# Kernel tuning notes

Hardware: AMD Instinct MI355X
Metric: run time of the kernel (lower is better)

Reference implementation:

```python
import jax, jax.numpy as jnp
import numpy as np
from jax import lax


def fps(xyz, npoints):
    """Furthest point sampling. xyz: [B,N,3] -> indices [B,npoints] (int32).
    Matches the standard PointNet++ CUDA kernel: first index is 0, then
    iteratively pick the point furthest from the selected set."""
    B, N, _ = xyz.shape
    first = jnp.zeros((B,), jnp.int32)
    d0 = jnp.sum((xyz - xyz[:, :1]) ** 2, axis=-1)  # [B,N] dist^2 to point 0

    def body(dists, _):
        idx = jnp.argmax(dists, axis=-1).astype(jnp.int32)  # [B]
        p = jnp.take_along_axis(xyz, idx[:, None, None].astype(jnp.int32), axis=1)  # [B,1,3]
        d = jnp.sum((xyz - p) ** 2, axis=-1)  # [B,N]
        return jnp.minimum(dists, d), idx

    _, idxs = lax.scan(body, d0, None, length=npoints - 1)  # [npoints-1, B]
    return jnp.concatenate([first[None, :], idxs], axis=0).T  # [B, npoints]


def pointwise_mlp(x, w1, b1, w2, b2):
    # shared per-point MLP (stand-in for PointNet2SemSegSSGShape encoder)
    h = jax.nn.relu(jnp.einsum('bnc,cf->bnf', x, w1) + b1)
    return jnp.einsum('bnf,fg->bng', h, w2) + b2


def _level(points, npoints, w1, b1, w2, b2, repeat):
    # downSample: FPS on xyz (first 3 channels), gather full feature rows
    idx = fps(lax.stop_gradient(points[:, :, :3]), npoints)  # [B,npoints]
    down = jnp.take_along_axis(points, idx[:, :, None], axis=1)  # [B,npoints,C]
    inp = jnp.concatenate([down, down], axis=-1) if repeat else down
    feat = pointwise_mlp(inp, w1, b1, w2, b2)  # [B,npoints,feat_dim]
    # concat xyz with feat channels 3: (matches original cat + transpose)
    return jnp.concatenate([down[:, :, :3], feat[:, :, 3:]], axis=-1)


def setup_inputs() -> dict:
    key = jax.random.key(0)
    ks = jax.random.split(key, 17)
    B, N = 8, 8192
    scene_points = jax.random.normal(ks[0], (B, N, 3), jnp.float32)
    # encoder channel plan: (in_ch, feat_dim) per level
    plan = [(6, 16), (16, 32), (32, 64), (64, 128)]
    out = {'scene_points': scene_points}
    k = 1
    for li, (cin, f) in enumerate(plan, start=1):
        s1 = 1.0 / np.sqrt(cin)
        s2 = 1.0 / np.sqrt(f)
        out[f'w1_{li}'] = jax.random.normal(ks[k], (cin, f), jnp.float32) * s1; k += 1
        out[f'b1_{li}'] = jnp.zeros((f,), jnp.float32)
        out[f'w2_{li}'] = jax.random.normal(ks[k], (f, f), jnp.float32) * s2; k += 1
        out[f'b2_{li}'] = jnp.zeros((f,), jnp.float32)
    return out


def reference(scene_points,
              w1_1, b1_1, w2_1, b2_1,
              w1_2, b1_2, w2_2, b2_2,
              w1_3, b1_3, w2_3, b2_3,
              w1_4, b1_4, w2_4, b2_4):
    B, N, _ = scene_points.shape
    f1 = _level(scene_points, N // 2, w1_1, b1_1, w2_1, b2_1, repeat=True)
    f2 = _level(f1, N // 4, w1_2, b1_2, w2_2, b2_2, repeat=False)
    f3 = _level(f2, N // 8, w1_3, b1_3, w2_3, b2_3, repeat=False)
    f4 = _level(f3, N // 16, w1_4, b1_4, w2_4, b2_4, repeat=False)
    return (f1, f2, f3, f4)
```

## Files before the change

### kernel.cpp

```cpp
#include <hip/hip_runtime.h>

typedef float f32x2 __attribute__((ext_vector_type(2)));

__device__ __forceinline__ f32x2 pk_add(f32x2 a, f32x2 b) {
    f32x2 d; asm("v_pk_add_f32 %0, %1, %2" : "=v"(d) : "v"(a), "v"(b)); return d;
}
__device__ __forceinline__ f32x2 pk_mul(f32x2 a, f32x2 b) {
    f32x2 d; asm("v_pk_mul_f32 %0, %1, %2" : "=v"(d) : "v"(a), "v"(b)); return d;
}
__device__ __forceinline__ f32x2 pk_fma(f32x2 a, f32x2 b, f32x2 c) {
    f32x2 d; asm("v_pk_fma_f32 %0, %1, %2, %3" : "=v"(d) : "v"(a), "v"(b), "v"(c)); return d;
}

__device__ __forceinline__ double dist2d(float x, float y, float z,
                                         double px, double py, double pz) {
    double dx = __dsub_rn((double)x, px);
    double dy = __dsub_rn((double)y, py);
    double dz = __dsub_rn((double)z, pz);
    double a  = __dmul_rn(dx, dx);
    double b  = __dmul_rn(dy, dy);
    double c  = __dmul_rn(dz, dz);
    return __dadd_rn(__dadd_rn(a, b), c);
}

template <int CTRL>
__device__ __forceinline__ unsigned dpp_u32_keep(unsigned v) {
    return (unsigned)__builtin_amdgcn_update_dpp((int)v, (int)v, CTRL, 0xF, 0xF, false);
}

__device__ __forceinline__ unsigned wave_umax64(unsigned v) {
    v = max(v, dpp_u32_keep<0x111>(v));
    v = max(v, dpp_u32_keep<0x112>(v));
    v = max(v, dpp_u32_keep<0x114>(v));
    v = max(v, dpp_u32_keep<0x118>(v));
    v = max(v, dpp_u32_keep<0x142>(v));
    v = max(v, dpp_u32_keep<0x143>(v));
    return v;
}

__device__ __forceinline__ float readlane_f32(float v, int l) {
    return __int_as_float(__builtin_amdgcn_readlane(__float_as_int(v), l));
}

template <int PPT, int NT>
__global__ __launch_bounds__(NT, 4) void fps_kernel(
    const float* __restrict__ pts,
    int stride, int npoints,
    int* __restrict__ idx_out)
{
    constexpr int NWAVES = NT / 64;
    constexpr int N_IN   = PPT * NT;
    constexpr int NPAIR  = PPT / 2;
    constexpr int LOGNT  = (NT == 1024) ? 10 : (NT == 512) ? 9 : 8;

    const int batch = blockIdx.x;
    const int tid   = threadIdx.x;
    const int lane  = tid & 63;
    const int wv    = tid >> 6;

    const float* base = pts + (size_t)batch * N_IN * stride;
    int* iout = idx_out + (size_t)batch * npoints;

    __shared__ uint2  s_pk[2][NWAVES];
    __shared__ float4 s_c[2][NWAVES];
    __shared__ int    s_hist[4096];

    f32x2  pcx[NPAIR], pcy[NPAIR], pcz[NPAIR];
    double md[PPT];
    float  th[PPT];

#pragma unroll
    for (int k = 0; k < NPAIR; ++k) {
        int p0 = (2 * k) * NT + tid;
        int p1 = (2 * k + 1) * NT + tid;
        const float* r0 = base + (size_t)p0 * stride;
        const float* r1 = base + (size_t)p1 * stride;
        pcx[k] = f32x2{r0[0], r1[0]};
        pcy[k] = f32x2{r0[1], r1[1]};
        pcz[k] = f32x2{r0[2], r1[2]};
    }

    float q0x = base[0], q0y = base[1], q0z = base[2];
    if (tid == 0) s_hist[0] = 0;

    double bv = -1.0;
    int    bj = 0;
    float  bx = 0.f, by = 0.f, bz = 0.f;
#pragma unroll
    for (int j = 0; j < PPT; ++j) {
        float x = pcx[j / 2][j & 1], y = pcy[j / 2][j & 1], z = pcz[j / 2][j & 1];
        md[j] = dist2d(x, y, z, (double)q0x, (double)q0y, (double)q0z);
        th[j] = __fmul_rn((float)md[j], 1.000004f);
        if (md[j] > bv) { bv = md[j]; bj = j; bx = x; by = y; bz = z; }
    }

    unsigned w_hi = 0, w_lo = 0;
    int      w_i  = 0;
    float    w_x = 0.f, w_y = 0.f, w_z = 0.f;
    bool pub0 = false, pub1 = false;

    auto reduce_winner = [&]() {
        unsigned hi = (unsigned)__double2hiint(bv);
        unsigned lo = (unsigned)__double2loint(bv);
        int      bi = (bj << LOGNT) + tid;
        unsigned maxhi = (unsigned)__builtin_amdgcn_readlane((int)wave_umax64(hi), 63);
        unsigned long long cm = __ballot(hi == maxhi);
        int wl;
        if (__popcll(cm) == 1) {
            wl = __ffsll(cm) - 1;
        } else {
            unsigned bl = 0; int bidx = 0x7FFFFFFF; int ml = -1;
            unsigned long long t2 = cm;
            while (t2) {
                int l = __ffsll(t2) - 1;
                unsigned lol = (unsigned)__builtin_amdgcn_readlane((int)lo, l);
                int      il  = __builtin_amdgcn_readlane(bi, l);
                if (ml < 0 || lol > bl || (lol == bl && il < bidx)) {
                    bl = lol; bidx = il; ml = l;
                }
                t2 &= t2 - 1;
            }
            wl = ml;
        }
        w_hi = maxhi;
        w_lo = (unsigned)__builtin_amdgcn_readlane((int)lo, wl);
        w_i  = __builtin_amdgcn_readlane(bi, wl);
        w_x  = readlane_f32(bx, wl);
        w_y  = readlane_f32(by, wl);
        w_z  = readlane_f32(bz, wl);
        pub0 = false; pub1 = false;
    };
    reduce_winner();

    for (int i = 1; i < npoints; ++i) {
        const int par = i & 1;

        bool pub = par ? pub1 : pub0;
        if (!pub) {
            if (lane == 0) {
                s_pk[par][wv] = make_uint2(w_hi, (unsigned)w_i);
                s_c[par][wv]  = make_float4(w_x, w_y, w_z, __uint_as_float(w_lo));
            }
            if (par) pub1 = true; else pub0 = true;
        }
        __syncthreads();

        const int sl = lane & (NWAVES - 1);
        uint2  pk = s_pk[par][sl];
        float4 pc = s_c[par][sl];
        unsigned v2 = (lane < NWAVES) ? pk.x : 0u;
        v2 = max(v2, dpp_u32_keep<0x111>(v2));
        v2 = max(v2, dpp_u32_keep<0x112>(v2));
        if constexpr (NWAVES >= 8)  v2 = max(v2, dpp_u32_keep<0x114>(v2));
        if constexpr (NWAVES >= 16) v2 = max(v2, dpp_u32_keep<0x118>(v2));
        unsigned ghi = (unsigned)__builtin_amdgcn_readlane((int)v2, NWAVES - 1);
        unsigned long long c2 = __ballot((lane < NWAVES) && (pk.x == ghi));
        int wl2;
        if (__popcll(c2) == 1) {
            wl2 = __ffsll(c2) - 1;
        } else {
            unsigned bl = 0; int bidx = 0x7FFFFFFF; int ml = -1;
            unsigned long long t2 = c2;
            while (t2) {
                int l = __ffsll(t2) - 1;
                unsigned lol = (unsigned)__builtin_amdgcn_readlane(__float_as_int(pc.w), l);
                int      il  = __builtin_amdgcn_readlane((int)pk.y, l);
                if (ml < 0 || lol > bl || (lol == bl && il < bidx)) {
                    bl = lol; bidx = il; ml = l;
                }
                t2 &= t2 - 1;
            }
            wl2 = ml;
        }
        int best = __builtin_amdgcn_readlane((int)pk.y, wl2);
        if (tid == 0) s_hist[i] = best;

        const float qx = readlane_f32(pc.x, wl2);
        const float qy = readlane_f32(pc.y, wl2);
        const float qz = readlane_f32(pc.z, wl2);
        const double qx64 = (double)qx, qy64 = (double)qy, qz64 = (double)qz;

        const f32x2 nqx = {-qx, -qx}, nqy = {-qy, -qy}, nqz = {-qz, -qz};
        int fmask = 0;
#pragma unroll
        for (int k = 0; k < NPAIR; ++k) {
            f32x2 dx = pk_add(pcx[k], nqx);
            f32x2 dy = pk_add(pcy[k], nqy);
            f32x2 dz = pk_add(pcz[k], nqz);
            f32x2 d  = pk_fma(dx, dx, pk_fma(dy, dy, pk_mul(dz, dz)));
            fmask |= (__any(d.x < th[2 * k])     ? (1 << (2 * k))     : 0);
            fmask |= (__any(d.y < th[2 * k + 1]) ? (1 << (2 * k + 1)) : 0);
        }

        if (fmask) {
            bool need = false;
#pragma unroll
            for (int j = 0; j < PPT; ++j) {
                if (fmask & (1 << j)) {
                    float x = pcx[j / 2][j & 1], y = pcy[j / 2][j & 1], z = pcz[j / 2][j & 1];
                    double d   = dist2d(x, y, z, qx64, qy64, qz64);
                    double old = md[j];
                    need = need | ((bj == j) & (d < old));
                    md[j] = fmin(old, d);
                    th[j] = __fmul_rn((float)md[j], 1.000004f);
                }
            }
            if (__any(need)) {
                bv = -1.0; bj = 0;
#pragma unroll
                for (int j = 0; j < PPT; ++j) {
                    if (md[j] > bv) {
                        bv = md[j]; bj = j;
                        bx = pcx[j / 2][j & 1]; by = pcy[j / 2][j & 1]; bz = pcz[j / 2][j & 1];
                    }
                }
                reduce_winner();
            }
        }
    }

    __syncthreads();
    for (int i = tid; i < npoints; i += NT) iout[i] = s_hist[i];
}

template <int CIN, int F, bool REPEAT, bool IDENT>
__global__ __launch_bounds__(256) void mlp_kernel(
    const float* __restrict__ pts, int stride, int n_in,
    const int* __restrict__ idx,
    const float* __restrict__ w1, const float* __restrict__ b1,
    const float* __restrict__ w2, const float* __restrict__ b2,
    float* __restrict__ out, int np)
{
    constexpr int P    = 256 / F;
    constexpr int CINS = REPEAT ? (CIN / 2) : CIN;
    constexpr int LOGF = (F == 16) ? 4 : (F == 32) ? 5 : (F == 64) ? 6 : 7;

    __shared__ float xs[P][CINS];
    __shared__ float h[P][F];

    const int tid = threadIdx.x;
    const int pl  = tid >> LOGF;
    const int c   = tid & (F - 1);
    const int b   = blockIdx.y;
    const int pid = blockIdx.x * P + pl;

    const int id = IDENT ? pid : idx[(size_t)b * np + pid];
    const float* row = pts + ((size_t)b * n_in + id) * stride;

    if (c < CINS) xs[pl][c] = row[c];
    __syncthreads();

    float acc = b1[c];
#pragma unroll
    for (int k = 0; k < CIN; ++k) {
        const int xk = REPEAT ? (k % 3) : k;
        acc = fmaf(xs[pl][xk], w1[k * F + c], acc);
    }
    h[pl][c] = fmaxf(acc, 0.0f);
    __syncthreads();

    float acc2 = b2[c];
#pragma unroll
    for (int f = 0; f < F; ++f)
        acc2 = fmaf(h[pl][f], w2[f * F + c], acc2);

    float res = (c < 3) ? xs[pl][c] : acc2;
    out[((size_t)b * np + pid) * (size_t)F + c] = res;
}

extern "C" void kernel_launch(void* const* d_in, const int* in_sizes, int n_in_cnt,
                              void* d_out, int out_size, void* d_ws, size_t ws_size,
                              hipStream_t stream) {
    const float* scene = (const float*)d_in[0];
    const float* w1_1 = (const float*)d_in[1];
    const float* b1_1 = (const float*)d_in[2];
    const float* w2_1 = (const float*)d_in[3];
    const float* b2_1 = (const float*)d_in[4];
    const float* w1_2 = (const float*)d_in[5];
    const float* b1_2 = (const float*)d_in[6];
    const float* w2_2 = (const float*)d_in[7];
    const float* b2_2 = (const float*)d_in[8];
    const float* w1_3 = (const float*)d_in[9];
    const float* b1_3 = (const float*)d_in[10];
    const float* w2_3 = (const float*)d_in[11];
    const float* b2_3 = (const float*)d_in[12];
    const float* w1_4 = (const float*)d_in[13];
    const float* b1_4 = (const float*)d_in[14];
    const float* w2_4 = (const float*)d_in[15];
    const float* b2_4 = (const float*)d_in[16];

    float* out  = (float*)d_out;
    float* out1 = out;
    float* out2 = out + 524288;
    float* out3 = out + 1048576;
    float* out4 = out + 1572864;

    int* idx1 = (int*)d_ws;

    const int B = 8;

    fps_kernel<8, 1024><<<B, 1024, 0, stream>>>(scene, 3, 4096, idx1);
    mlp_kernel<6, 16, true, false><<<dim3(256, B), 256, 0, stream>>>(
        scene, 3, 8192, idx1, w1_1, b1_1, w2_1, b2_1, out1, 4096);

    mlp_kernel<16, 32, false, true><<<dim3(256, B), 256, 0, stream>>>(
        out1, 16, 4096, nullptr, w1_2, b1_2, w2_2, b2_2, out2, 2048);

    mlp_kernel<32, 64, false, true><<<dim3(256, B), 256, 0, stream>>>(
        out2, 32, 2048, nullptr, w1_3, b1_3, w2_3, b2_3, out3, 1024);

    mlp_kernel<64, 128, false, true><<<dim3(256, B), 256, 0, stream>>>(
        out3, 64, 1024, nullptr, w1_4, b1_4, w2_4, b2_4, out4, 512);
}
```

Before: 5.095 ms.

## Track top-two candidates to commit two FPS picks per barrier

Each thread and wave now tracks its best and second-best distances. The block reduction produces both the global winner and a runner-up. When the runner-up is no further from the first pick than its own current distance, it must be the next FPS choice, so two points are committed in one iteration with a single __syncthreads. This halves barriers and reductions on favourable steps, at the cost of extra top-2 scans, larger shared-memory publishes and a second update pass.

```diff
diff --git a/kernel.cpp b/kernel.cpp
--- a/kernel.cpp
+++ b/kernel.cpp
@@ -40,6 +40,20 @@
 
 __device__ __forceinline__ float readlane_f32(float v, int l) {
     return __int_as_float(__builtin_amdgcn_readlane(__float_as_int(v), l));
+}
+
+__device__ __forceinline__ int pick_lane(unsigned long long m, unsigned lo, int idx) {
+    if (__popcll(m) == 1) return __ffsll(m) - 1;
+    unsigned bl = 0; int bidx = 0x7FFFFFFF; int ml = -1;
+    unsigned long long t = m;
+    while (t) {
+        int l = __ffsll(t) - 1;
+        unsigned lol = (unsigned)__builtin_amdgcn_readlane((int)lo, l);
+        int      il  = __builtin_amdgcn_readlane(idx, l);
+        if (ml < 0 || lol > bl || (lol == bl && il < bidx)) { bl = lol; bidx = il; ml = l; }
+        t &= t - 1;
+    }
+    return ml;
 }
 
 template <int PPT, int NT>
@@ -61,8 +75,9 @@
     const float* base = pts + (size_t)batch * N_IN * stride;
     int* iout = idx_out + (size_t)batch * npoints;
 
-    __shared__ uint2  s_pk[2][NWAVES];
-    __shared__ float4 s_c[2][NWAVES];
+    __shared__ uint4  s_pk[2][NWAVES];
+    __shared__ float4 s_c1[2][NWAVES];
+    __shared__ float4 s_c2[2][NWAVES];
     __shared__ int    s_hist[4096];
 
     f32x2  pcx[NPAIR], pcy[NPAIR], pcz[NPAIR];
@@ -83,144 +98,173 @@
     float q0x = base[0], q0y = base[1], q0z = base[2];
     if (tid == 0) s_hist[0] = 0;
 
-    double bv = -1.0;
-    int    bj = 0;
-    float  bx = 0.f, by = 0.f, bz = 0.f;
 #pragma unroll
     for (int j = 0; j < PPT; ++j) {
         float x = pcx[j / 2][j & 1], y = pcy[j / 2][j & 1], z = pcz[j / 2][j & 1];
         md[j] = dist2d(x, y, z, (double)q0x, (double)q0y, (double)q0z);
         th[j] = __fmul_rn((float)md[j], 1.000004f);
-        if (md[j] > bv) { bv = md[j]; bj = j; bx = x; by = y; bz = z; }
-    }
-
-    unsigned w_hi = 0, w_lo = 0;
-    int      w_i  = 0;
-    float    w_x = 0.f, w_y = 0.f, w_z = 0.f;
+    }
+
+    double bv = -1.0, b2v = -1.0;
+    int    bj = 0,    b2j = 0;
+    float  bx = 0.f, by = 0.f, bz = 0.f;
+    float  b2x = 0.f, b2y = 0.f, b2z = 0.f;
+
+    auto scan12 = [&]() {
+        bv = -1.0; bj = 0;
+#pragma unroll
+        for (int j = 0; j < PPT; ++j) {
+            float x = pcx[j / 2][j & 1], y = pcy[j / 2][j & 1], z = pcz[j / 2][j & 1];
+            if (md[j] > bv) { bv = md[j]; bj = j; bx = x; by = y; bz = z; }
+        }
+        b2v = -1.0; b2j = 0;
+#pragma unroll
+        for (int j = 0; j < PPT; ++j) {
+            float x = pcx[j / 2][j & 1], y = pcy[j / 2][j & 1], z = pcz[j / 2][j & 1];
+            if ((j != bj) && (md[j] > b2v)) { b2v = md[j]; b2j = j; b2x = x; b2y = y; b2z = z; }
+        }
+    };
+
+    unsigned w1hi = 0, w1lo = 0, w2hi = 0, w2lo = 0;
+    int      w1i = 0, w2i = 0;
+    float    w1x = 0.f, w1y = 0.f, w1z = 0.f, w2x = 0.f, w2y = 0.f, w2z = 0.f;
     bool pub0 = false, pub1 = false;
 
     auto reduce_winner = [&]() {
-        unsigned hi = (unsigned)__double2hiint(bv);
-        unsigned lo = (unsigned)__double2loint(bv);
-        int      bi = (bj << LOGNT) + tid;
-        unsigned maxhi = (unsigned)__builtin_amdgcn_readlane((int)wave_umax64(hi), 63);
-        unsigned long long cm = __ballot(hi == maxhi);
-        int wl;
-        if (__popcll(cm) == 1) {
-            wl = __ffsll(cm) - 1;
-        } else {
-            unsigned bl = 0; int bidx = 0x7FFFFFFF; int ml = -1;
-            unsigned long long t2 = cm;
-            while (t2) {
-                int l = __ffsll(t2) - 1;
-                unsigned lol = (unsigned)__builtin_amdgcn_readlane((int)lo, l);
-                int      il  = __builtin_amdgcn_readlane(bi, l);
-                if (ml < 0 || lol > bl || (lol == bl && il < bidx)) {
-                    bl = lol; bidx = il; ml = l;
-                }
-                t2 &= t2 - 1;
-            }
-            wl = ml;
-        }
-        w_hi = maxhi;
-        w_lo = (unsigned)__builtin_amdgcn_readlane((int)lo, wl);
-        w_i  = __builtin_amdgcn_readlane(bi, wl);
-        w_x  = readlane_f32(bx, wl);
-        w_y  = readlane_f32(by, wl);
-        w_z  = readlane_f32(bz, wl);
+        unsigned hi1  = (unsigned)__double2hiint(bv);
+        unsigned lo1  = (unsigned)__double2loint(bv);
+        int      idx1 = (bj << LOGNT) + tid;
+        unsigned mx1 = (unsigned)__builtin_amdgcn_readlane((int)wave_umax64(hi1), 63);
+        int wl = pick_lane(__ballot(hi1 == mx1), lo1, idx1);
+        w1hi = mx1;
+        w1lo = (unsigned)__builtin_amdgcn_readlane((int)lo1, wl);
+        w1i  = __builtin_amdgcn_readlane(idx1, wl);
+        w1x  = readlane_f32(bx, wl);
+        w1y  = readlane_f32(by, wl);
+        w1z  = readlane_f32(bz, wl);
+        bool sel = (lane == wl);
+        unsigned mh  = sel ? (unsigned)__double2hiint(b2v) : hi1;
+        unsigned mlo = sel ? (unsigned)__double2loint(b2v) : lo1;
+        int      mix = sel ? ((b2j << LOGNT) + tid) : idx1;
+        float    mxx = sel ? b2x : bx;
+        float    myy = sel ? b2y : by;
+        float    mzz = sel ? b2z : bz;
+        unsigned mx2 = (unsigned)__builtin_amdgcn_readlane((int)wave_umax64(mh), 63);
+        int wl2 = pick_lane(__ballot(mh == mx2), mlo, mix);
+        w2hi = mx2;
+        w2lo = (unsigned)__builtin_amdgcn_readlane((int)mlo, wl2);
+        w2i  = __builtin_amdgcn_readlane(mix, wl2);
+        w2x  = readlane_f32(mxx, wl2);
+        w2y  = readlane_f32(myy, wl2);
+        w2z  = readlane_f32(mzz, wl2);
         pub0 = false; pub1 = false;
     };
+
+    scan12();
     reduce_winner();
 
-    for (int i = 1; i < npoints; ++i) {
-        const int par = i & 1;
-
-        bool pub = par ? pub1 : pub0;
-        if (!pub) {
+    int i = 1, cv = 0;
+    while (i < npoints) {
+        const int par = cv & 1;
+        ++cv;
+
+        bool pubd = par ? pub1 : pub0;
+        if (!pubd) {
             if (lane == 0) {
-                s_pk[par][wv] = make_uint2(w_hi, (unsigned)w_i);
-                s_c[par][wv]  = make_float4(w_x, w_y, w_z, __uint_as_float(w_lo));
+                s_pk[par][wv] = make_uint4(w1hi, (unsigned)w1i, w2hi, (unsigned)w2i);
+                s_c1[par][wv] = make_float4(w1x, w1y, w1z, __uint_as_float(w1lo));
+                s_c2[par][wv] = make_float4(w2x, w2y, w2z, __uint_as_float(w2lo));
             }
             if (par) pub1 = true; else pub0 = true;
         }
         __syncthreads();
 
         const int sl = lane & (NWAVES - 1);
-        uint2  pk = s_pk[par][sl];
-        float4 pc = s_c[par][sl];
-        unsigned v2 = (lane < NWAVES) ? pk.x : 0u;
+        uint4  pk = s_pk[par][sl];
+        float4 c1 = s_c1[par][sl];
+        float4 c2 = s_c2[par][sl];
+
+        unsigned v1 = (lane < NWAVES) ? pk.x : 0u;
+        v1 = max(v1, dpp_u32_keep<0x111>(v1));
+        v1 = max(v1, dpp_u32_keep<0x112>(v1));
+        if constexpr (NWAVES >= 8)  v1 = max(v1, dpp_u32_keep<0x114>(v1));
+        if constexpr (NWAVES >= 16) v1 = max(v1, dpp_u32_keep<0x118>(v1));
+        unsigned ghi1 = (unsigned)__builtin_amdgcn_readlane((int)v1, NWAVES - 1);
+        int wlA = pick_lane(__ballot((lane < NWAVES) && (pk.x == ghi1)),
+                            (unsigned)__float_as_int(c1.w), (int)pk.y);
+        int   i1  = __builtin_amdgcn_readlane((int)pk.y, wlA);
+        float q1x = readlane_f32(c1.x, wlA);
+        float q1y = readlane_f32(c1.y, wlA);
+        float q1z = readlane_f32(c1.z, wlA);
+        unsigned g1lo = (unsigned)__builtin_amdgcn_readlane(__float_as_int(c1.w), wlA);
+
+        bool msel = (sl == wlA);
+        unsigned mh  = msel ? pk.z : pk.x;
+        int      mix = (int)(msel ? pk.w : pk.y);
+        float    mlw = msel ? c2.w : c1.w;
+        unsigned mlo = (unsigned)__float_as_int(mlw);
+        float    mqx = msel ? c2.x : c1.x;
+        float    mqy = msel ? c2.y : c1.y;
+        float    mqz = msel ? c2.z : c1.z;
+        unsigned v2 = (lane < NWAVES) ? mh : 0u;
         v2 = max(v2, dpp_u32_keep<0x111>(v2));
         v2 = max(v2, dpp_u32_keep<0x112>(v2));
         if constexpr (NWAVES >= 8)  v2 = max(v2, dpp_u32_keep<0x114>(v2));
         if constexpr (NWAVES >= 16) v2 = max(v2, dpp_u32_keep<0x118>(v2));
-        unsigned ghi = (unsigned)__builtin_amdgcn_readlane((int)v2, NWAVES - 1);
-        unsigned long long c2 = __ballot((lane < NWAVES) && (pk.x == ghi));
-        int wl2;
-        if (__popcll(c2) == 1) {
-            wl2 = __ffsll(c2) - 1;
-        } else {
-            unsigned bl = 0; int bidx = 0x7FFFFFFF; int ml = -1;
-            unsigned long long t2 = c2;
-            while (t2) {
-                int l = __ffsll(t2) - 1;
-                unsigned lol = (unsigned)__builtin_amdgcn_readlane(__float_as_int(pc.w), l);
-                int      il  = __builtin_amdgcn_readlane((int)pk.y, l);
-                if (ml < 0 || lol > bl || (lol == bl && il < bidx)) {
-                    bl = lol; bidx = il; ml = l;
-                }
-                t2 &= t2 - 1;
+        unsigned ghi2 = (unsigned)__builtin_amdgcn_readlane((int)v2, NWAVES - 1);
+        int wlB = pick_lane(__ballot((lane < NWAVES) && (mh == ghi2)), mlo, mix);
+        int   i2  = __builtin_amdgcn_readlane(mix, wlB);
+        float q2x = readlane_f32(mqx, wlB);
+        float q2y = readlane_f32(mqy, wlB);
+        float q2z = readlane_f32(mqz, wlB);
+        unsigned g2lo = (unsigned)__builtin_amdgcn_readlane((int)mlo, wlB);
+
+        const double q1x64 = (double)q1x, q1y64 = (double)q1y, q1z64 = (double)q1z;
+        double M2d = __hiloint2double((int)ghi2, (int)g2lo);
+        double d12 = dist2d(q2x, q2y, q2z, q1x64, q1y64, q1z64);
+        bool happy = (i + 1 < npoints) && (d12 >= M2d)
+                     && ((ghi1 | g1lo) != 0u) && ((ghi2 | g2lo) != 0u);
+
+        if (tid == 0) { s_hist[i] = i1; if (happy) s_hist[i + 1] = i2; }
+
+        bool need = false;
+        auto pass = [&](float qx, float qy, float qz) {
+            const double px = (double)qx, py = (double)qy, pz = (double)qz;
+            const f32x2 nqx = {-qx, -qx}, nqy = {-qy, -qy}, nqz = {-qz, -qz};
+            int fmask = 0;
+#pragma unroll
+            for (int k = 0; k < NPAIR; ++k) {
+                f32x2 dx = pk_add(pcx[k], nqx);
+                f32x2 dy = pk_add(pcy[k], nqy);
+                f32x2 dz = pk_add(pcz[k], nqz);
+                f32x2 d  = pk_fma(dx, dx, pk_fma(dy, dy, pk_mul(dz, dz)));
+                fmask |= (__any(d.x < th[2 * k])     ? (1 << (2 * k))     : 0);
+                fmask |= (__any(d.y < th[2 * k + 1]) ? (1 << (2 * k + 1)) : 0);
             }
-            wl2 = ml;
-        }
-        int best = __builtin_amdgcn_readlane((int)pk.y, wl2);
-        if (tid == 0) s_hist[i] = best;
-
-        const float qx = readlane_f32(pc.x, wl2);
-        const float qy = readlane_f32(pc.y, wl2);
-        const float qz = readlane_f32(pc.z, wl2);
-        const double qx64 = (double)qx, qy64 = (double)qy, qz64 = (double)qz;
-
-        const f32x2 nqx = {-qx, -qx}, nqy = {-qy, -qy}, nqz = {-qz, -qz};
-        int fmask = 0;
-#pragma unroll
-        for (int k = 0; k < NPAIR; ++k) {
-            f32x2 dx = pk_add(pcx[k], nqx);
-            f32x2 dy = pk_add(pcy[k], nqy);
-            f32x2 dz = pk_add(pcz[k], nqz);
-            f32x2 d  = pk_fma(dx, dx, pk_fma(dy, dy, pk_mul(dz, dz)));
-            fmask |= (__any(d.x < th[2 * k])     ? (1 << (2 * k))     : 0);
-            fmask |= (__any(d.y < th[2 * k + 1]) ? (1 << (2 * k + 1)) : 0);
-        }
-
-        if (fmask) {
-            bool need = false;
-#pragma unroll
-            for (int j = 0; j < PPT; ++j) {
-                if (fmask & (1 << j)) {
-                    float x = pcx[j / 2][j & 1], y = pcy[j / 2][j & 1], z = pcz[j / 2][j & 1];
-                    double d   = dist2d(x, y, z, qx64, qy64, qz64);
-                    double old = md[j];
-                    need = need | ((bj == j) & (d < old));
-                    md[j] = fmin(old, d);
-                    th[j] = __fmul_rn((float)md[j], 1.000004f);
+            if (fmask) {
+#pragma unroll
+                for (int j = 0; j < PPT; ++j) {
+                    if (fmask & (1 << j)) {
+                        float x = pcx[j / 2][j & 1], y = pcy[j / 2][j & 1], z = pcz[j / 2][j & 1];
+                        double d   = dist2d(x, y, z, px, py, pz);
+                        double old = md[j];
+                        need = need | (((bj == j) | (b2j == j)) & (d < old));
+                        md[j] = fmin(old, d);
+                        th[j] = __fmul_rn((float)md[j], 1.000004f);
+                    }
                 }
             }
-            if (__any(need)) {
-                bv = -1.0; bj = 0;
-#pragma unroll
-                for (int j = 0; j < PPT; ++j) {
-                    if (md[j] > bv) {
-                        bv = md[j]; bj = j;
-                        bx = pcx[j / 2][j & 1]; by = pcy[j / 2][j & 1]; bz = pcz[j / 2][j & 1];
-                    }
-                }
-                reduce_winner();
-            }
-        }
+        };
+        pass(q1x, q1y, q1z);
+        if (happy) pass(q2x, q2y, q2z);
+
+        if (__any(need)) { scan12(); reduce_winner(); }
+
+        i += happy ? 2 : 1;
     }
 
     __syncthreads();
-    for (int i = tid; i < npoints; i += NT) iout[i] = s_hist[i];
+    for (int k = tid; k < npoints; k += NT) iout[k] = s_hist[k];
 }
 
 template <int CIN, int F, bool REPEAT, bool IDENT>
```

Result: slower. 5.514 ms (+8.2%).

## Track per-thread top-two distances to avoid full rescans in FPS

Applied to the files above, without the earlier changes.

Each thread now keeps both its best and second-best candidate distances. When the best one shrinks, it either keeps the new value or promotes the runner-up, and only does a full rescan when neither is possible. The second-best list is rebuilt lazily, overlapped with the barrier. The wave winner is published straight from the winning lane and only when the best value changed, removing the per-iteration broadcast of winner state. This adds registers and branch logic in exchange for fewer full PPT-wide rescans in the serial FPS loop.

```diff
diff --git a/kernel.cpp b/kernel.cpp
--- a/kernel.cpp
+++ b/kernel.cpp
@@ -40,6 +40,20 @@
 
 __device__ __forceinline__ float readlane_f32(float v, int l) {
     return __int_as_float(__builtin_amdgcn_readlane(__float_as_int(v), l));
+}
+
+__device__ __forceinline__ int pick_lane(unsigned long long m, unsigned lo, int idx) {
+    if (__popcll(m) == 1) return __ffsll(m) - 1;
+    unsigned bl = 0; int bidx = 0x7FFFFFFF; int ml = -1;
+    unsigned long long t = m;
+    while (t) {
+        int l = __ffsll(t) - 1;
+        unsigned lol = (unsigned)__builtin_amdgcn_readlane((int)lo, l);
+        int      il  = __builtin_amdgcn_readlane(idx, l);
+        if (ml < 0 || lol > bl || (lol == bl && il < bidx)) { bl = lol; bidx = il; ml = l; }
+        t &= t - 1;
+    }
+    return ml;
 }
 
 template <int PPT, int NT>
@@ -83,101 +97,118 @@
     float q0x = base[0], q0y = base[1], q0z = base[2];
     if (tid == 0) s_hist[0] = 0;
 
-    double bv = -1.0;
-    int    bj = 0;
-    float  bx = 0.f, by = 0.f, bz = 0.f;
 #pragma unroll
     for (int j = 0; j < PPT; ++j) {
         float x = pcx[j / 2][j & 1], y = pcy[j / 2][j & 1], z = pcz[j / 2][j & 1];
         md[j] = dist2d(x, y, z, (double)q0x, (double)q0y, (double)q0z);
         th[j] = __fmul_rn((float)md[j], 1.000004f);
-        if (md[j] > bv) { bv = md[j]; bj = j; bx = x; by = y; bz = z; }
-    }
-
-    unsigned w_hi = 0, w_lo = 0;
-    int      w_i  = 0;
-    float    w_x = 0.f, w_y = 0.f, w_z = 0.f;
-    bool pub0 = false, pub1 = false;
-
-    auto reduce_winner = [&]() {
-        unsigned hi = (unsigned)__double2hiint(bv);
-        unsigned lo = (unsigned)__double2loint(bv);
-        int      bi = (bj << LOGNT) + tid;
-        unsigned maxhi = (unsigned)__builtin_amdgcn_readlane((int)wave_umax64(hi), 63);
-        unsigned long long cm = __ballot(hi == maxhi);
-        int wl;
-        if (__popcll(cm) == 1) {
-            wl = __ffsll(cm) - 1;
-        } else {
-            unsigned bl = 0; int bidx = 0x7FFFFFFF; int ml = -1;
-            unsigned long long t2 = cm;
-            while (t2) {
-                int l = __ffsll(t2) - 1;
-                unsigned lol = (unsigned)__builtin_amdgcn_readlane((int)lo, l);
-                int      il  = __builtin_amdgcn_readlane(bi, l);
-                if (ml < 0 || lol > bl || (lol == bl && il < bidx)) {
-                    bl = lol; bidx = il; ml = l;
-                }
-                t2 &= t2 - 1;
-            }
-            wl = ml;
-        }
-        w_hi = maxhi;
-        w_lo = (unsigned)__builtin_amdgcn_readlane((int)lo, wl);
-        w_i  = __builtin_amdgcn_readlane(bi, wl);
-        w_x  = readlane_f32(bx, wl);
-        w_y  = readlane_f32(by, wl);
-        w_z  = readlane_f32(bz, wl);
-        pub0 = false; pub1 = false;
+    }
+
+    double bv = -1.0, b2v = -1.0;
+    int    bj = 0,    b2j = 0;
+    float  bx = 0.f, by = 0.f, bz = 0.f;
+    float  b2x = 0.f, b2y = 0.f, b2z = 0.f;
+    bool   dirty = false;
+
+    auto scan12 = [&]() {
+        bv = -1.0; bj = 0;
+#pragma unroll
+        for (int j = 0; j < PPT; ++j) {
+            float x = pcx[j / 2][j & 1], y = pcy[j / 2][j & 1], z = pcz[j / 2][j & 1];
+            if (md[j] > bv) { bv = md[j]; bj = j; bx = x; by = y; bz = z; }
+        }
+        b2v = -1.0; b2j = 0;
+#pragma unroll
+        for (int j = 0; j < PPT; ++j) {
+            float x = pcx[j / 2][j & 1], y = pcy[j / 2][j & 1], z = pcz[j / 2][j & 1];
+            if ((j != bj) && (md[j] > b2v)) { b2v = md[j]; b2j = j; b2x = x; b2y = y; b2z = z; }
+        }
+        dirty = false;
     };
-    reduce_winner();
+
+    auto rebuild2 = [&]() {
+        b2v = -1.0; b2j = 0;
+#pragma unroll
+        for (int j = 0; j < PPT; ++j) {
+            float x = pcx[j / 2][j & 1], y = pcy[j / 2][j & 1], z = pcz[j / 2][j & 1];
+            if ((j != bj) && (md[j] > b2v)) { b2v = md[j]; b2j = j; b2x = x; b2y = y; b2z = z; }
+        }
+        dirty = false;
+    };
+
+    bool pubA = false, pubB = false;
+    bool iwrote = false;
+
+    auto wave_reduce_publish = [&](int wp) {
+        unsigned hi  = (unsigned)__double2hiint(bv);
+        unsigned lo  = (unsigned)__double2loint(bv);
+        int      idx = (bj << LOGNT) + tid;
+        unsigned mx  = (unsigned)__builtin_amdgcn_readlane((int)wave_umax64(hi), 63);
+        int wl = pick_lane(__ballot(hi == mx), lo, idx);
+        iwrote = (lane == wl);
+        if (iwrote) {
+            s_pk[wp][wv] = make_uint2(hi, (unsigned)idx);
+            s_c[wp][wv]  = make_float4(bx, by, bz, __uint_as_float(lo));
+        }
+    };
+
+    scan12();
+    {
+        unsigned hi  = (unsigned)__double2hiint(bv);
+        unsigned lo  = (unsigned)__double2loint(bv);
+        int      idx = (bj << LOGNT) + tid;
+        unsigned mx  = (unsigned)__builtin_amdgcn_readlane((int)wave_umax64(hi), 63);
+        int wl = pick_lane(__ballot(hi == mx), lo, idx);
+        iwrote = (lane == wl);
+        if (iwrote) {
+            s_pk[0][wv] = make_uint2(hi, (unsigned)idx);
+            s_c[0][wv]  = make_float4(bx, by, bz, __uint_as_float(lo));
+            s_pk[1][wv] = s_pk[0][wv];
+            s_c[1][wv]  = s_c[0][wv];
+        }
+        pubA = true; pubB = true;
+    }
 
     for (int i = 1; i < npoints; ++i) {
         const int par = i & 1;
 
-        bool pub = par ? pub1 : pub0;
-        if (!pub) {
-            if (lane == 0) {
-                s_pk[par][wv] = make_uint2(w_hi, (unsigned)w_i);
-                s_c[par][wv]  = make_float4(w_x, w_y, w_z, __uint_as_float(w_lo));
+        bool pubCur = par ? pubB : pubA;
+        if (!pubCur) {
+            if (iwrote) {
+                unsigned hi  = (unsigned)__double2hiint(bv);
+                unsigned lo  = (unsigned)__double2loint(bv);
+                int      idx = (bj << LOGNT) + tid;
+                s_pk[par][wv] = make_uint2(hi, (unsigned)idx);
+                s_c[par][wv]  = make_float4(bx, by, bz, __uint_as_float(lo));
             }
-            if (par) pub1 = true; else pub0 = true;
+            if (par) pubB = true; else pubA = true;
         }
         __syncthreads();
 
-        const int sl = lane & (NWAVES - 1);
-        uint2  pk = s_pk[par][sl];
-        float4 pc = s_c[par][sl];
-        unsigned v2 = (lane < NWAVES) ? pk.x : 0u;
+        unsigned phi = 0u, pidx = 0u;
+        float pqx = 0.f, pqy = 0.f, pqz = 0.f, plo = 0.f;
+        if (lane < NWAVES) {
+            uint2  pk = s_pk[par][lane];
+            float4 pc = s_c[par][lane];
+            phi = pk.x; pidx = pk.y;
+            pqx = pc.x; pqy = pc.y; pqz = pc.z; plo = pc.w;
+        }
+        if (__any(dirty)) { if (dirty) rebuild2(); }
+
+        unsigned v2 = phi;
         v2 = max(v2, dpp_u32_keep<0x111>(v2));
         v2 = max(v2, dpp_u32_keep<0x112>(v2));
         if constexpr (NWAVES >= 8)  v2 = max(v2, dpp_u32_keep<0x114>(v2));
         if constexpr (NWAVES >= 16) v2 = max(v2, dpp_u32_keep<0x118>(v2));
         unsigned ghi = (unsigned)__builtin_amdgcn_readlane((int)v2, NWAVES - 1);
-        unsigned long long c2 = __ballot((lane < NWAVES) && (pk.x == ghi));
-        int wl2;
-        if (__popcll(c2) == 1) {
-            wl2 = __ffsll(c2) - 1;
-        } else {
-            unsigned bl = 0; int bidx = 0x7FFFFFFF; int ml = -1;
-            unsigned long long t2 = c2;
-            while (t2) {
-                int l = __ffsll(t2) - 1;
-                unsigned lol = (unsigned)__builtin_amdgcn_readlane(__float_as_int(pc.w), l);
-                int      il  = __builtin_amdgcn_readlane((int)pk.y, l);
-                if (ml < 0 || lol > bl || (lol == bl && il < bidx)) {
-                    bl = lol; bidx = il; ml = l;
-                }
-                t2 &= t2 - 1;
-            }
-            wl2 = ml;
-        }
-        int best = __builtin_amdgcn_readlane((int)pk.y, wl2);
+        int wl2 = pick_lane(__ballot((lane < NWAVES) && (phi == ghi)),
+                            (unsigned)__float_as_int(plo), (int)pidx);
+        int best = __builtin_amdgcn_readlane((int)pidx, wl2);
         if (tid == 0) s_hist[i] = best;
 
-        const float qx = readlane_f32(pc.x, wl2);
-        const float qy = readlane_f32(pc.y, wl2);
-        const float qz = readlane_f32(pc.z, wl2);
+        const float qx = readlane_f32(pqx, wl2);
+        const float qy = readlane_f32(pqy, wl2);
+        const float qz = readlane_f32(pqz, wl2);
         const double qx64 = (double)qx, qy64 = (double)qy, qz64 = (double)qz;
 
         const f32x2 nqx = {-qx, -qx}, nqy = {-qy, -qy}, nqz = {-qz, -qz};
@@ -193,34 +224,41 @@
         }
 
         if (fmask) {
-            bool need = false;
+            bool decB = false, dec2 = false;
+            double dNew = 0.0;
 #pragma unroll
             for (int j = 0; j < PPT; ++j) {
                 if (fmask & (1 << j)) {
                     float x = pcx[j / 2][j & 1], y = pcy[j / 2][j & 1], z = pcz[j / 2][j & 1];
                     double d   = dist2d(x, y, z, qx64, qy64, qz64);
                     double old = md[j];
-                    need = need | ((bj == j) & (d < old));
+                    bool dj  = (d < old);
+                    bool isB = (bj == j) & dj;
+                    decB = decB | isB;
+                    dec2 = dec2 | ((b2j == j) & dj);
+                    dNew = isB ? d : dNew;
                     md[j] = fmin(old, d);
                     th[j] = __fmul_rn((float)md[j], 1.000004f);
                 }
             }
-            if (__any(need)) {
-                bv = -1.0; bj = 0;
-#pragma unroll
-                for (int j = 0; j < PPT; ++j) {
-                    if (md[j] > bv) {
-                        bv = md[j]; bj = j;
-                        bx = pcx[j / 2][j & 1]; by = pcy[j / 2][j & 1]; bz = pcz[j / 2][j & 1];
-                    }
-                }
-                reduce_winner();
+            bool full    = decB & (dec2 | (dNew == b2v));
+            bool promote = decB & !full & (dNew < b2v);
+            bool keep    = decB & !full & !promote;
+            if (promote) { bv = b2v; bj = b2j; bx = b2x; by = b2y; bz = b2z; dirty = true; }
+            if (keep)    { bv = dNew; }
+            dirty = dirty | (dec2 & !decB);
+            if (__any(full)) { if (full) scan12(); }
+
+            if (__any(decB)) {
+                wave_reduce_publish(par ^ 1);
+                if (par) { pubA = true; pubB = false; }
+                else     { pubB = true; pubA = false; }
             }
         }
     }
 
     __syncthreads();
-    for (int i = tid; i < npoints; i += NT) iout[i] = s_hist[i];
+    for (int k = tid; k < npoints; k += NT) iout[k] = s_hist[k];
 }
 
 template <int CIN, int F, bool REPEAT, bool IDENT>
```

Result: no change. 5.189 ms (+1.8%).
